# Kernel optimization log

Measured on AMD Instinct MI355X. Metric: run time of the kernel, lower is better.

Reference implementation:

```python
import jax, jax.numpy as jnp
import numpy as np

B, S, D_IN, D_E = 8, 2048, 1024, 1024


def setup_inputs() -> dict:
    key = jax.random.key(0)
    ks = jax.random.split(key, 9)
    s_in = 1.0 / np.sqrt(D_IN)
    s_e = 1.0 / np.sqrt(D_E)
    return {
        "x": jax.random.normal(ks[0], (B, S, D_IN), dtype=jnp.float32),
        "Wq": jax.random.uniform(ks[1], (D_IN, D_E), jnp.float32, -s_in, s_in),
        "bq": jax.random.uniform(ks[2], (D_E,), jnp.float32, -s_in, s_in),
        "Wk": jax.random.uniform(ks[3], (D_IN, D_E), jnp.float32, -s_in, s_in),
        "bk": jax.random.uniform(ks[4], (D_E,), jnp.float32, -s_in, s_in),
        "Wv": jax.random.uniform(ks[5], (D_IN, D_E), jnp.float32, -s_in, s_in),
        "bv": jax.random.uniform(ks[6], (D_E,), jnp.float32, -s_in, s_in),
        "Wo": jax.random.uniform(ks[7], (D_E, D_E), jnp.float32, -s_e, s_e),
        "bo": jax.random.uniform(ks[8], (D_E,), jnp.float32, -s_e, s_e),
    }


def reference(x, Wq, bq, Wk, bk, Wv, bv, Wo, bo):
    # QKV projections: [B,S,D_in] @ [D_in,D_e] -> [B,S,D_e]
    Q = jnp.einsum("bsi,ie->bse", x, Wq) + bq
    K = jnp.einsum("bsi,ie->bse", x, Wk) + bk
    V = jnp.einsum("bsi,ie->bse", x, Wv) + bv
    scale = 1.0 / jnp.sqrt(jnp.asarray(Q.shape[-1], Q.dtype))
    # full score matrix [B,S,S] (faithful to the unfused original)
    logits = jnp.einsum("bqe,bke->bqk", Q, K) * scale
    attn = jax.nn.softmax(logits, axis=-1)
    values = jnp.einsum("bqk,bke->bqe", attn, V)
    o = jnp.einsum("bqe,ef->bqf", values, Wo) + bo
    return o
```

## Files before the change

### kernel.cpp

```cpp
#include <hip/hip_runtime.h>

#define DIN 1024
#define DE  1024
#define SEQ 2048
#define NB  8

typedef __bf16 bf16x8 __attribute__((ext_vector_type(8)));
typedef float  f32x4  __attribute__((ext_vector_type(4)));
typedef unsigned short u16;
typedef u16 u16x8 __attribute__((ext_vector_type(8)));
typedef u16 u16x4 __attribute__((ext_vector_type(4)));

__device__ __forceinline__ u16 f2bf(float f) {
  unsigned u = __builtin_bit_cast(unsigned, f);
  return (u16)((u + 0x7FFFu + ((u >> 16) & 1u)) >> 16);
}
__device__ __forceinline__ float bf2f(u16 h) {
  return __builtin_bit_cast(float, (unsigned)h << 16);
}

typedef __attribute__((address_space(1))) const unsigned char g_u8;
typedef __attribute__((address_space(3))) unsigned char l_u8;
__device__ __forceinline__ void gload16(const void* g, void* l) {
  __builtin_amdgcn_global_load_lds((g_u8*)g, (l_u8*)l, 16, 0, 0);
}

__global__ __launch_bounds__(256) void cvt_f32_bf16(const float* __restrict__ in,
                                                    u16* __restrict__ out, int n4) {
  int i = blockIdx.x * 256 + threadIdx.x;
  if (i >= n4) return;
  float4 v = ((const float4*)in)[i];
  u16x4 o;
  o[0] = f2bf(v.x); o[1] = f2bf(v.y); o[2] = f2bf(v.z); o[3] = f2bf(v.w);
  ((u16x4*)out)[i] = o;
}

__global__ __launch_bounds__(256) void transpose_w(const float* __restrict__ W,
                                                   u16* __restrict__ Wt) {
  __shared__ float t[32][33];
  const int tx = threadIdx.x, ty = threadIdx.y;
  const int bx = blockIdx.x * 32, by = blockIdx.y * 32;
#pragma unroll
  for (int i = 0; i < 4; ++i)
    t[ty + i * 8][tx] = W[(size_t)(by + ty + i * 8) * 1024 + bx + tx];
  __syncthreads();
#pragma unroll
  for (int i = 0; i < 4; ++i)
    Wt[(size_t)(bx + ty + i * 8) * 1024 + by + tx] = f2bf(t[tx][ty + i * 8]);
}

__global__ __launch_bounds__(256) void softmax_rows_bf16(u16* __restrict__ P) {
  const size_t row = blockIdx.x;
  u16* pr = P + row * 2048 + (size_t)threadIdx.x * 8;
  u16x8 v = *(const u16x8*)pr;
  float x[8];
#pragma unroll
  for (int j = 0; j < 8; ++j) x[j] = bf2f(v[j]);
  float m = x[0];
#pragma unroll
  for (int j = 1; j < 8; ++j) m = fmaxf(m, x[j]);
#pragma unroll
  for (int off = 32; off; off >>= 1) m = fmaxf(m, __shfl_xor(m, off));
  __shared__ float rm[4], rs[4];
  const int lane = threadIdx.x & 63, wid = threadIdx.x >> 6;
  if (lane == 0) rm[wid] = m;
  __syncthreads();
  m = fmaxf(fmaxf(rm[0], rm[1]), fmaxf(rm[2], rm[3]));
  float s = 0.f;
#pragma unroll
  for (int j = 0; j < 8; ++j) { x[j] = __expf(x[j] - m); s += x[j]; }
#pragma unroll
  for (int off = 32; off; off >>= 1) s += __shfl_xor(s, off);
  if (lane == 0) rs[wid] = s;
  __syncthreads();
  s = (rs[0] + rs[1]) + (rs[2] + rs[3]);
  const float inv = 1.f / s;
  u16x8 o;
#pragma unroll
  for (int j = 0; j < 8; ++j) o[j] = f2bf(x[j] * inv);
  *(u16x8*)pr = o;
}

template <int BMT, int OMODE, bool HAS_BIAS>
__global__ __launch_bounds__(512, 1) void gemmph(
    const u16* __restrict__ A, const u16* __restrict__ Bt, void* __restrict__ Cv,
    const float* __restrict__ bias, int M, int N, int K,
    size_t sA, size_t sB, size_t sC, float scale) {
  constexpr int ABYTES = BMT * 128;
  constexpr int AHALF  = ABYTES / 2;
  constexpr int BUFB   = ABYTES + 32768;
  constexpr int LA     = AHALF / 8192;
  constexpr int MR     = BMT / 32;
  __shared__ __align__(16) char lds8[2 * BUFB];
  const int tid = threadIdx.x, lane = tid & 63, wid = tid >> 6;
  const int wm = wid >> 2, wn = wid & 3;
  const int lane15 = lane & 15, gk = lane >> 4;

  const int gx = gridDim.x, gy = gridDim.y;
  int lin = blockIdx.x + gx * (blockIdx.y + gy * blockIdx.z);
  const int nwg = gx * gy * (int)gridDim.z;
  const int q = nwg >> 3, r8 = nwg & 7;
  const int xcd = lin & 7, idx = lin >> 3;
  lin = (xcd < r8 ? xcd * (q + 1) : r8 * (q + 1) + (xcd - r8) * q) + idx;
  const int bz = lin / (gx * gy);
  const int rem = lin - bz * (gx * gy);
  const int by = rem / gx, bx = rem - (rem / gx) * gx;

  const char* Ag = (const char*)(A + (size_t)bz * sA + (size_t)by * BMT * K);
  const char* Bg = (const char*)(Bt + (size_t)bz * sB + (size_t)bx * 256 * K);
  const size_t Kb = (size_t)K * 2;

  const int spr = tid >> 3;
  const int sg = (tid & 7) ^ (spr & 7);
  const char* srcA[2][2];
  const char* srcB[2][2];
#pragma unroll
  for (int h = 0; h < 2; ++h) {
#pragma unroll
    for (int j = 0; j < LA; ++j)
      srcA[h][j] = Ag + (size_t)(h * (BMT / 2) + j * 64 + spr) * Kb + sg * 16;
#pragma unroll
    for (int j = 0; j < 2; ++j)
      srcB[h][j] = Bg + (size_t)(h * 128 + j * 64 + spr) * Kb + sg * 16;
  }

  auto stageA2 = [&](int dbuf) {
#pragma unroll
    for (int h = 0; h < 2; ++h) {
      char* d = lds8 + dbuf * BUFB + h * AHALF + tid * 16;
#pragma unroll
      for (int j = 0; j < LA; ++j) { gload16(srcA[h][j], d + j * 8192); srcA[h][j] += 128; }
    }
  };
  auto stageB1 = [&](int h, int dbuf) {
    char* d = lds8 + dbuf * BUFB + ABYTES + h * 16384 + tid * 16;
    gload16(srcB[h][0], d);        srcB[h][0] += 128;
    gload16(srcB[h][1], d + 8192); srcB[h][1] += 128;
  };

  const int arow = lane15 * 128 + ((gk ^ (lane15 & 7)) << 4);

  f32x4 acc[MR][4] = {};
  const int NT = K >> 6;

  stageA2(0); stageB1(0, 0); stageB1(1, 0);
  stageB1(0, 1); stageA2(1);
  if constexpr (BMT == 256) asm volatile("s_waitcnt vmcnt(6)" ::: "memory");
  else                      asm volatile("s_waitcnt vmcnt(4)" ::: "memory");
  __builtin_amdgcn_s_barrier();
  __builtin_amdgcn_sched_barrier(0);

  for (int kt = 0; kt < NT; ++kt) {
    const char* Ab = lds8 + (kt & 1) * BUFB + wm * AHALF;
    const char* Bb = lds8 + (kt & 1) * BUFB + ABYTES + (wn >> 1) * 16384 + (wn & 1) * 8192;
    const int nbuf = (kt + 1) & 1;
    const int cbuf = kt & 1;
    bf16x8 af[4][2], bfr[4][2];

    if constexpr (BMT == 256) {
#pragma unroll
      for (int m = 0; m < 4; ++m) {
        af[m][0] = *(const bf16x8*)(Ab + m * 2048 + arow);
        af[m][1] = *(const bf16x8*)(Ab + m * 2048 + (arow ^ 64));
      }
#pragma unroll
      for (int n = 0; n < 2; ++n) {
        bfr[n][0] = *(const bf16x8*)(Bb + n * 2048 + arow);
        bfr[n][1] = *(const bf16x8*)(Bb + n * 2048 + (arow ^ 64));
      }
      if (kt + 1 < NT) stageB1(1, nbuf);
      __builtin_amdgcn_s_barrier();
      asm volatile("s_waitcnt lgkmcnt(0)" ::: "memory");
      __builtin_amdgcn_sched_barrier(0);
      __builtin_amdgcn_s_setprio(1);
#pragma unroll
      for (int m = 0; m < 4; ++m)
#pragma unroll
        for (int n = 0; n < 2; ++n) {
          acc[m][n] = __builtin_amdgcn_mfma_f32_16x16x32_bf16(af[m][0], bfr[n][0], acc[m][n], 0, 0, 0);
          acc[m][n] = __builtin_amdgcn_mfma_f32_16x16x32_bf16(af[m][1], bfr[n][1], acc[m][n], 0, 0, 0);
        }
      __builtin_amdgcn_s_setprio(0);
      __builtin_amdgcn_s_barrier();
      __builtin_amdgcn_sched_barrier(0);
#pragma unroll
      for (int n = 2; n < 4; ++n) {
        bfr[n][0] = *(const bf16x8*)(Bb + n * 2048 + arow);
        bfr[n][1] = *(const bf16x8*)(Bb + n * 2048 + (arow ^ 64));
      }
      __builtin_amdgcn_s_barrier();
      asm volatile("s_waitcnt lgkmcnt(0)" ::: "memory");
      __builtin_amdgcn_sched_barrier(0);
      __builtin_amdgcn_s_setprio(1);
#pragma unroll
      for (int m = 0; m < 4; ++m)
#pragma unroll
        for (int n = 2; n < 4; ++n) {
          acc[m][n] = __builtin_amdgcn_mfma_f32_16x16x32_bf16(af[m][0], bfr[n][0], acc[m][n], 0, 0, 0);
          acc[m][n] = __builtin_amdgcn_mfma_f32_16x16x32_bf16(af[m][1], bfr[n][1], acc[m][n], 0, 0, 0);
        }
      __builtin_amdgcn_s_setprio(0);
      __builtin_amdgcn_s_barrier();
      __builtin_amdgcn_sched_barrier(0);
#pragma unroll
      for (int m = 0; m < 4; ++m) {
        af[m][0] = *(const bf16x8*)(Ab + (4 + m) * 2048 + arow);
        af[m][1] = *(const bf16x8*)(Ab + (4 + m) * 2048 + (arow ^ 64));
      }
      if (kt + 2 < NT) stageB1(0, cbuf);
      __builtin_amdgcn_s_barrier();
      asm volatile("s_waitcnt lgkmcnt(0)" ::: "memory");
      __builtin_amdgcn_sched_barrier(0);
      __builtin_amdgcn_s_setprio(1);
#pragma unroll
      for (int m = 0; m < 4; ++m)
#pragma unroll
        for (int n = 0; n < 2; ++n) {
          acc[4 + m][n] = __builtin_amdgcn_mfma_f32_16x16x32_bf16(af[m][0], bfr[n][0], acc[4 + m][n], 0, 0, 0);
          acc[4 + m][n] = __builtin_amdgcn_mfma_f32_16x16x32_bf16(af[m][1], bfr[n][1], acc[4 + m][n], 0, 0, 0);
        }
      __builtin_amdgcn_s_setprio(0);
      __builtin_amdgcn_s_barrier();
      __builtin_amdgcn_sched_barrier(0);
      if (kt + 2 < NT) stageA2(cbuf);
      __builtin_amdgcn_s_barrier();
      asm volatile("s_waitcnt lgkmcnt(0)" ::: "memory");
      __builtin_amdgcn_sched_barrier(0);
      __builtin_amdgcn_s_setprio(1);
#pragma unroll
      for (int m = 0; m < 4; ++m)
#pragma unroll
        for (int n = 2; n < 4; ++n) {
          acc[4 + m][n] = __builtin_amdgcn_mfma_f32_16x16x32_bf16(af[m][0], bfr[n][0], acc[4 + m][n], 0, 0, 0);
          acc[4 + m][n] = __builtin_amdgcn_mfma_f32_16x16x32_bf16(af[m][1], bfr[n][1], acc[4 + m][n], 0, 0, 0);
        }
      __builtin_amdgcn_s_setprio(0);
      if (kt < NT - 2)      asm volatile("s_waitcnt vmcnt(6)" ::: "memory");
      else if (kt == NT - 2) asm volatile("s_waitcnt vmcnt(0)" ::: "memory");
      __builtin_amdgcn_s_barrier();
      __builtin_amdgcn_sched_barrier(0);
    } else {
#pragma unroll
      for (int m = 0; m < 4; ++m) {
        af[m][0] = *(const bf16x8*)(Ab + m * 2048 + arow);
        af[m][1] = *(const bf16x8*)(Ab + m * 2048 + (arow ^ 64));
      }
#pragma unroll
      for (int n = 0; n < 4; ++n) {
        bfr[n][0] = *(const bf16x8*)(Bb + n * 2048 + arow);
        bfr[n][1] = *(const bf16x8*)(Bb + n * 2048 + (arow ^ 64));
      }
      if (kt + 1 < NT) stageB1(1, nbuf);
      __builtin_amdgcn_s_barrier();
      asm volatile("s_waitcnt lgkmcnt(0)" ::: "memory");
      __builtin_amdgcn_sched_barrier(0);
      __builtin_amdgcn_s_setprio(1);
#pragma unroll
      for (int m = 0; m < 4; ++m)
#pragma unroll
        for (int n = 0; n < 2; ++n) {
          acc[m][n] = __builtin_amdgcn_mfma_f32_16x16x32_bf16(af[m][0], bfr[n][0], acc[m][n], 0, 0, 0);
          acc[m][n] = __builtin_amdgcn_mfma_f32_16x16x32_bf16(af[m][1], bfr[n][1], acc[m][n], 0, 0, 0);
        }
      __builtin_amdgcn_s_setprio(0);
      __builtin_amdgcn_s_barrier();
      __builtin_amdgcn_sched_barrier(0);
      if (kt + 2 < NT) { stageA2(cbuf); stageB1(0, cbuf); }
      __builtin_amdgcn_s_barrier();
      asm volatile("s_waitcnt lgkmcnt(0)" ::: "memory");
      __builtin_amdgcn_sched_barrier(0);
      __builtin_amdgcn_s_setprio(1);
#pragma unroll
      for (int m = 0; m < 4; ++m)
#pragma unroll
        for (int n = 2; n < 4; ++n) {
          acc[m][n] = __builtin_amdgcn_mfma_f32_16x16x32_bf16(af[m][0], bfr[n][0], acc[m][n], 0, 0, 0);
          acc[m][n] = __builtin_amdgcn_mfma_f32_16x16x32_bf16(af[m][1], bfr[n][1], acc[m][n], 0, 0, 0);
        }
      __builtin_amdgcn_s_setprio(0);
      if (kt < NT - 2)      asm volatile("s_waitcnt vmcnt(4)" ::: "memory");
      else if (kt == NT - 2) asm volatile("s_waitcnt vmcnt(0)" ::: "memory");
      __builtin_amdgcn_s_barrier();
      __builtin_amdgcn_sched_barrier(0);
    }
  }

  const int rbase = by * BMT + wm * (BMT / 2) + (gk << 2);
  const int cbase = bx * 256 + wn * 64 + lane15;
#pragma unroll
  for (int m = 0; m < MR; ++m)
#pragma unroll
    for (int n = 0; n < 4; ++n) {
      const int col = cbase + n * 16;
      const float bval = HAS_BIAS ? bias[col] : 0.f;
#pragma unroll
      for (int r = 0; r < 4; ++r) {
        const int rowg = rbase + m * 16 + r;
        const float v = acc[m][n][r] * scale + bval;
        if (OMODE == 0)
          ((float*)Cv)[(size_t)bz * sC + (size_t)rowg * N + col] = v;
        else if (OMODE == 1)
          ((u16*)Cv)[(size_t)bz * sC + (size_t)rowg * N + col] = f2bf(v);
        else
          ((u16*)Cv)[(size_t)(rowg >> 11) * ((size_t)DE * SEQ) +
                     (size_t)col * SEQ + (rowg & 2047)] = f2bf(v);
      }
    }
}

extern "C" void kernel_launch(void* const* d_in, const int* in_sizes, int n_in,
                              void* d_out, int out_size, void* d_ws, size_t ws_size,
                              hipStream_t stream) {
  const float* x  = (const float*)d_in[0];
  const float* Wq = (const float*)d_in[1];
  const float* bq = (const float*)d_in[2];
  const float* Wk = (const float*)d_in[3];
  const float* bk = (const float*)d_in[4];
  const float* Wv = (const float*)d_in[5];
  const float* bv = (const float*)d_in[6];
  const float* Wo = (const float*)d_in[7];
  const float* bo = (const float*)d_in[8];

  const size_t NEED = 150994944;
  if (ws_size < NEED) return;
  char* ws = (char*)d_ws;
  u16* x_bf = (u16*)(ws);
  u16* q_bf = (u16*)(ws + 33554432);
  u16* k_bf = (u16*)(ws + 67108864);
  u16* vt   = (u16*)(ws + 100663296);
  u16* wt   = (u16*)(ws + 134217728);
  u16* lgP  = x_bf;
  u16* wt_q = wt;
  u16* wt_k = wt + 1048576;
  u16* wt_v = wt + 2097152;
  u16* wt_o = wt + 3145728;

  dim3 tb(32, 8);
  const size_t sQ = (size_t)SEQ * DE;
  const size_t sL = (size_t)1024 * SEQ;

  cvt_f32_bf16<<<16384, 256, 0, stream>>>(x, x_bf, (NB * SEQ * DIN) / 4);
  transpose_w<<<dim3(32, 32), tb, 0, stream>>>(Wq, wt_q);
  transpose_w<<<dim3(32, 32), tb, 0, stream>>>(Wk, wt_k);
  transpose_w<<<dim3(32, 32), tb, 0, stream>>>(Wv, wt_v);
  transpose_w<<<dim3(32, 32), tb, 0, stream>>>(Wo, wt_o);
  gemmph<256, 1, true><<<dim3(4, 64, 1), 512, 0, stream>>>(x_bf, wt_q, q_bf, bq,
      16384, 1024, 1024, 0, 0, 0, 1.f);
  gemmph<256, 1, true><<<dim3(4, 64, 1), 512, 0, stream>>>(x_bf, wt_k, k_bf, bk,
      16384, 1024, 1024, 0, 0, 0, 1.f);
  gemmph<256, 2, true><<<dim3(4, 64, 1), 512, 0, stream>>>(x_bf, wt_v, vt, bv,
      16384, 1024, 1024, 0, 0, 0, 1.f);
  for (int c = 0; c < 2; ++c) {
    const u16* qc = q_bf + (size_t)c * 1048576;
    gemmph<128, 1, false><<<dim3(8, 8, 8), 512, 0, stream>>>(qc, k_bf, lgP, nullptr,
        1024, 2048, 1024, sQ, sQ, sL, 0.03125f);
    softmax_rows_bf16<<<8192, 256, 0, stream>>>(lgP);
    gemmph<128, 1, false><<<dim3(4, 8, 8), 512, 0, stream>>>(lgP, vt,
        q_bf + (size_t)c * 1048576, nullptr, 1024, 1024, 2048, sL, sQ, sQ, 1.f);
  }
  gemmph<256, 0, true><<<dim3(4, 64, 1), 512, 0, stream>>>(q_bf, wt_o, d_out, bo,
      16384, 1024, 1024, 0, 0, 0, 1.f);

  (void)in_sizes; (void)n_in; (void)out_size; (void)ws_size;
}
```

Measured before the change: 376.6 us.

## Add 128x128 triple-buffered bf16 GEMM for attention score and PV products

Adds a new 256-thread GEMM kernel with 128x128 output tiles, a K-step of 32, a three-stage LDS ring filled by direct global-to-LDS loads, a swizzled LDS layout and XCD-aware block remapping. It replaces the 512-thread gemmph calls for QK^T and PV. The goal is more workgroups and better latency hiding on these mid-sized batched GEMMs. The trade-offs are smaller per-block reuse and scalar (uncoalesced-ish) bf16 stores in the epilogue.

```diff
diff --git a/kernel.cpp b/kernel.cpp
--- a/kernel.cpp
+++ b/kernel.cpp
@@ -79,6 +79,110 @@
 #pragma unroll
   for (int j = 0; j < 8; ++j) o[j] = f2bf(x[j] * inv);
   *(u16x8*)pr = o;
+}
+
+__global__ __launch_bounds__(256) void gemm2b(
+    const u16* __restrict__ A, const u16* __restrict__ Bt, u16* __restrict__ C,
+    int M, int N, int K, size_t sA, size_t sB, size_t sC, float scale) {
+  constexpr int BUF = 16384;
+  __shared__ __align__(16) char lds[3 * BUF];
+  const int tid = threadIdx.x, lane = tid & 63, wid = tid >> 6;
+  const int wm = wid >> 1, wn = wid & 1;
+  const int lane15 = lane & 15, gk = lane >> 4;
+
+  const int gx = gridDim.x, gy = gridDim.y;
+  int lin = blockIdx.x + gx * (blockIdx.y + gy * blockIdx.z);
+  const int nwg = gx * gy * (int)gridDim.z;
+  const int q = nwg >> 3, r8 = nwg & 7;
+  const int xcd = lin & 7, idx = lin >> 3;
+  lin = (xcd < r8 ? xcd * (q + 1) : r8 * (q + 1) + (xcd - r8) * q) + idx;
+  const int bz = lin / (gx * gy);
+  const int rem = lin - bz * (gx * gy);
+  const int by = rem / gx, bx = rem - (rem / gx) * gx;
+
+  const char* Ag = (const char*)(A + (size_t)bz * sA + (size_t)by * 128 * K);
+  const char* Bg = (const char*)(Bt + (size_t)bz * sB + (size_t)bx * 128 * K);
+  const size_t Kb = (size_t)K * 2;
+
+  const char* sa[2];
+  const char* sb[2];
+  int doff[2];
+#pragma unroll
+  for (int j = 0; j < 2; ++j) {
+    const int S = j * 256 + tid, pr = S >> 2, ps = S & 3;
+    const int g = ps ^ ((pr >> 1) & 3);
+    sa[j] = Ag + (size_t)pr * Kb + g * 16;
+    sb[j] = Bg + (size_t)pr * Kb + g * 16;
+    doff[j] = S * 16;
+  }
+
+  int aoff[4], boff[4];
+#pragma unroll
+  for (int m = 0; m < 4; ++m) {
+    const int r = wm * 64 + m * 16 + lane15;
+    aoff[m] = r * 64 + ((gk ^ ((r >> 1) & 3)) << 4);
+  }
+#pragma unroll
+  for (int n = 0; n < 4; ++n) {
+    const int r = wn * 64 + n * 16 + lane15;
+    boff[n] = 8192 + r * 64 + ((gk ^ ((r >> 1) & 3)) << 4);
+  }
+
+  f32x4 acc[4][4] = {};
+  const int NT = K >> 5;
+
+  auto stage = [&](int b) {
+    char* base = lds + b * BUF;
+#pragma unroll
+    for (int j = 0; j < 2; ++j) {
+      gload16(sa[j], base + doff[j]);
+      gload16(sb[j], base + 8192 + doff[j]);
+      sa[j] += 64; sb[j] += 64;
+    }
+  };
+
+  stage(0); stage(1);
+  asm volatile("s_waitcnt vmcnt(4)" ::: "memory");
+  __builtin_amdgcn_s_barrier();
+  __builtin_amdgcn_sched_barrier(0);
+
+  int cur = 0;
+  for (int t = 0; t < NT; ++t) {
+    if (t + 2 < NT) stage(cur == 0 ? 2 : cur - 1);
+    const char* base = lds + cur * BUF;
+    bf16x8 af[4], bfv[4];
+#pragma unroll
+    for (int m = 0; m < 4; ++m) af[m] = *(const bf16x8*)(base + aoff[m]);
+#pragma unroll
+    for (int n = 0; n < 4; ++n) bfv[n] = *(const bf16x8*)(base + boff[n]);
+    asm volatile("s_waitcnt lgkmcnt(0)" ::: "memory");
+    __builtin_amdgcn_sched_barrier(0);
+    __builtin_amdgcn_s_setprio(1);
+#pragma unroll
+    for (int m = 0; m < 4; ++m)
+#pragma unroll
+      for (int n = 0; n < 4; ++n)
+        acc[m][n] = __builtin_amdgcn_mfma_f32_16x16x32_bf16(af[m], bfv[n], acc[m][n], 0, 0, 0);
+    __builtin_amdgcn_s_setprio(0);
+    if (t < NT - 2)       asm volatile("s_waitcnt vmcnt(4)" ::: "memory");
+    else if (t == NT - 2) asm volatile("s_waitcnt vmcnt(0)" ::: "memory");
+    __builtin_amdgcn_s_barrier();
+    __builtin_amdgcn_sched_barrier(0);
+    cur = cur == 2 ? 0 : cur + 1;
+  }
+
+  const int rbase = by * 128 + wm * 64 + (gk << 2);
+  const int cbase = bx * 128 + wn * 64 + lane15;
+  u16* Cb = C + (size_t)bz * sC;
+#pragma unroll
+  for (int m = 0; m < 4; ++m)
+#pragma unroll
+    for (int n = 0; n < 4; ++n) {
+      const int col = cbase + n * 16;
+#pragma unroll
+      for (int r = 0; r < 4; ++r)
+        Cb[(size_t)(rbase + m * 16 + r) * N + col] = f2bf(acc[m][n][r] * scale);
+    }
 }
 
 template <int BMT, int OMODE, bool HAS_BIAS>
@@ -352,11 +456,11 @@
       16384, 1024, 1024, 0, 0, 0, 1.f);
   for (int c = 0; c < 2; ++c) {
     const u16* qc = q_bf + (size_t)c * 1048576;
-    gemmph<128, 1, false><<<dim3(8, 8, 8), 512, 0, stream>>>(qc, k_bf, lgP, nullptr,
+    gemm2b<<<dim3(16, 8, 8), 256, 0, stream>>>(qc, k_bf, lgP,
         1024, 2048, 1024, sQ, sQ, sL, 0.03125f);
     softmax_rows_bf16<<<8192, 256, 0, stream>>>(lgP);
-    gemmph<128, 1, false><<<dim3(4, 8, 8), 512, 0, stream>>>(lgP, vt,
-        q_bf + (size_t)c * 1048576, nullptr, 1024, 1024, 2048, sL, sQ, sQ, 1.f);
+    gemm2b<<<dim3(8, 8, 8), 256, 0, stream>>>(lgP, vt, q_bf + (size_t)c * 1048576,
+        1024, 1024, 2048, sL, sQ, sQ, 1.f);
   }
   gemmph<256, 0, true><<<dim3(4, 64, 1), 512, 0, stream>>>(q_bf, wt_o, d_out, bo,
       16384, 1024, 1024, 0, 0, 0, 1.f);
```

Result: no change. 378.2 us (+0.4%).
